# Kernel tuning notes

Measured on AMD Instinct MI355X. Metric: run time of the kernel, lower is better.

## Reference

```python
import jax, jax.numpy as jnp
import numpy as np


def setup_inputs() -> dict:
    key = jax.random.key(0)
    k1, k2 = jax.random.split(key)
    B, S, D, E = 4, 4096, 2048, 64
    x = jax.random.normal(k1, (B, S, D), dtype=jnp.float32)
    gate_w = jax.random.normal(k2, (E, D), dtype=jnp.float32) * (1.0 / np.sqrt(D))
    return {"x": x, "gate_w": gate_w, "top_k": 2}


def reference(x, gate_w, top_k):
    # logits = x @ W^T : [B, S, E]
    logits = jnp.einsum("bsd,ed->bse", x, gate_w)
    probs = jax.nn.softmax(logits, axis=-1)
    top_k_probs, top_k_indices = jax.lax.top_k(probs, top_k)
    top_k_probs = top_k_probs / jnp.sum(top_k_probs, axis=-1, keepdims=True)
    return (top_k_probs, top_k_indices, probs)
```

## Files before the change

### kernel.cpp

```cpp
#include <hip/hip_runtime.h>
#include <math.h>


typedef _Float16 half8  __attribute__((ext_vector_type(8)));
typedef float    floatx4 __attribute__((ext_vector_type(4)));

#define NTOK  16384
#define DDIM  2048
#define NE    64

__device__ inline void split8(const float4& a, const float4& b,
                              half8& hi, half8& lo) {
    float f[8] = {a.x, a.y, a.z, a.w, b.x, b.y, b.z, b.w};
#pragma unroll
    for (int j = 0; j < 8; ++j) {
        const _Float16 h = (_Float16)f[j];
        hi[j] = h;
        lo[j] = (_Float16)(f[j] - (float)h);
    }
}

__global__ __launch_bounds__(256) void w_split2(const float* __restrict__ W,
                                                _Float16* __restrict__ img) {
    const int g  = blockIdx.x * 256 + threadIdx.x;
    const int L  = g & 63;
    const int Bk = g >> 6;
    const int h  = Bk & 1;
    const int nt = (Bk >> 1) & 3;
    const int ch = (Bk >> 3) & 1;
    const int gs = Bk >> 4;
    const int c  = L & 15, q = L >> 4;
    const float* src = W + (size_t)(nt * 16 + c) * DDIM
                         + gs * 64 + ch * 32 + q * 8;
    const float4 a = *(const float4*)(src);
    const float4 b = *(const float4*)(src + 4);
    half8 hi, lo;
    split8(a, b, hi, lo);
    *(half8*)(img + (size_t)g * 8) = h ? lo : hi;
}

__global__ __launch_bounds__(256, 3) void router_mfma(
    const float* __restrict__ x,
    const _Float16* __restrict__ img,
    float* __restrict__ out)
{
    __shared__ __align__(16) float lg[4 * 16 * 68];

    const int tid = threadIdx.x;
    const int L   = tid & 63;
    const int kq  = __builtin_amdgcn_readfirstlane(tid >> 6);
    const int c   = L & 15, q = L >> 4;
    const int btok = blockIdx.x * 16;

    const float*    xp = x + (size_t)(btok + c) * DDIM + kq * 512 + q * 8;
    const _Float16* wp = img + (size_t)kq * 65536 + (size_t)L * 8;

    floatx4 acc[4];
#pragma unroll
    for (int nt = 0; nt < 4; ++nt) acc[nt] = (floatx4)0.f;

    float4 xA[4], xB[4];

    auto LX = [&](int s, float4* xb) {
#pragma unroll
        for (int ch = 0; ch < 2; ++ch) {
            xb[2 * ch + 0] = *(const float4*)(xp + s * 64 + ch * 32);
            xb[2 * ch + 1] = *(const float4*)(xp + s * 64 + ch * 32 + 4);
        }
    };
    auto LW = [&](int s, half8* wb) {
#pragma unroll
        for (int f = 0; f < 16; ++f)
            wb[f] = *(const half8*)(wp + (size_t)s * 8192 + f * 512);
    };
    auto CP = [&](const float4* xb, const half8* wb) {
#pragma unroll
        for (int ch = 0; ch < 2; ++ch) {
            half8 Ah, Al;
            split8(xb[2 * ch], xb[2 * ch + 1], Ah, Al);
#pragma unroll
            for (int nt = 0; nt < 4; ++nt) {
                const half8 Bh = wb[ch * 8 + nt * 2];
                const half8 Bl = wb[ch * 8 + nt * 2 + 1];
                acc[nt] = __builtin_amdgcn_mfma_f32_16x16x32_f16(Ah, Bh, acc[nt], 0, 0, 0);
                acc[nt] = __builtin_amdgcn_mfma_f32_16x16x32_f16(Al, Bh, acc[nt], 0, 0, 0);
                acc[nt] = __builtin_amdgcn_mfma_f32_16x16x32_f16(Ah, Bl, acc[nt], 0, 0, 0);
            }
        }
    };

    LX(0, xA);
    LX(1, xB);
#pragma unroll 1
    for (int b = 0; b < 6; b += 2) {
        half8 wA[16], wB[16];
        LW(b, wA);
        CP(xA, wA);
        LX(b + 2, xA);
        LW(b + 1, wB);
        CP(xB, wB);
        LX(b + 3, xB);
    }
    {
        half8 wA[16], wB[16];
        LW(6, wA); CP(xA, wA);
        LW(7, wB); CP(xB, wB);
    }

    {
        float* slab = &lg[kq * 16 * 68];
#pragma unroll
        for (int nt = 0; nt < 4; ++nt)
#pragma unroll
            for (int r = 0; r < 4; ++r)
                slab[(q * 4 + r) * 68 + nt * 16 + c] = acc[nt][r];
    }
    __syncthreads();

#pragma unroll
    for (int i = 0; i < 4; ++i) {
        const int e = tid + 256 * i;
        const int r = e >> 6, col = e & 63;
        const int o = r * 68 + col;
        lg[o] = (lg[o] + lg[1088 + o]) + (lg[2176 + o] + lg[3264 + o]);
    }
    __syncthreads();

    if (tid < 16) {
        const int token = btok + tid;
        float* row = &lg[tid * 68];
        float pr[NE];
#pragma unroll
        for (int e = 0; e < NE; ++e) pr[e] = row[e];

        float m = pr[0];
#pragma unroll
        for (int e = 1; e < NE; ++e) m = fmaxf(m, pr[e]);
        float s = 0.f;
#pragma unroll
        for (int e = 0; e < NE; ++e) { pr[e] = expf(pr[e] - m); s += pr[e]; }
        const float inv = 1.f / s;

        float v1 = -1.f; int i1 = 0;
#pragma unroll
        for (int e = 0; e < NE; ++e) { if (pr[e] > v1) { v1 = pr[e]; i1 = e; } }
        float v2 = -1.f; int i2 = 0;
#pragma unroll
        for (int e = 0; e < NE; ++e) { if (e != i1 && pr[e] > v2) { v2 = pr[e]; i2 = e; } }

        const float ts = v1 + v2;
        float* out_tp = out;
        float* out_ti = out + 2 * NTOK;
        *(float2*)(out_tp + token * 2) = make_float2(v1 / ts, v2 / ts);
        *(float2*)(out_ti + token * 2) = make_float2((float)i1, (float)i2);

#pragma unroll
        for (int e = 0; e < NE; ++e) row[e] = pr[e] * inv;
    }
    __syncthreads();

    {
        float* out_p = out + 4 * NTOK + (size_t)btok * NE;
        const int r = tid >> 4, c4 = tid & 15;
        const float4 v = *(const float4*)&lg[r * 68 + 4 * c4];
        *(float4*)(out_p + tid * 4) = v;
    }
}

extern "C" void kernel_launch(void* const* d_in, const int* in_sizes, int n_in,
                              void* d_out, int out_size, void* d_ws, size_t ws_size,
                              hipStream_t stream) {
    const float* x = (const float*)d_in[0];
    const float* W = (const float*)d_in[1];
    float* out     = (float*)d_out;
    _Float16* img  = (_Float16*)d_ws;

    w_split2<<<dim3(128), dim3(256), 0, stream>>>(W, img);
    router_mfma<<<dim3(NTOK / 16), dim3(256), 0, stream>>>(x, img, out);
}
```

Measured before the change: 206.1 us.

## Fuse weight split into router kernel with LDS double-buffered 32-token tiles

Removes the separate weight-split pre-kernel. Each block now loads fp32 W and x slices from global memory per K-step, splits them into fp16 hi/lo parts, and stages them in double-buffered LDS. The block grows to 512 threads covering 32 tokens, with each wave owning one 16x16 output tile, so the cross-wave K-reduction through shared memory goes away. In exchange, every block re-reads and re-splits all of W, and each K-step pays a block-wide barrier with little prefetch depth.

```diff
diff --git a/kernel.cpp b/kernel.cpp
--- a/kernel.cpp
+++ b/kernel.cpp
@@ -3,11 +3,14 @@
 
 
 typedef _Float16 half8  __attribute__((ext_vector_type(8)));
+typedef _Float16 half4  __attribute__((ext_vector_type(4)));
 typedef float    floatx4 __attribute__((ext_vector_type(4)));
 
 #define NTOK  16384
 #define DDIM  2048
 #define NE    64
+#define TPB   32
+#define NSTEP 32
 
 __device__ inline void split8(const float4& a, const float4& b,
                               half8& hi, half8& lo) {
@@ -20,113 +23,103 @@
     }
 }
 
-__global__ __launch_bounds__(256) void w_split2(const float* __restrict__ W,
-                                                _Float16* __restrict__ img) {
-    const int g  = blockIdx.x * 256 + threadIdx.x;
-    const int L  = g & 63;
-    const int Bk = g >> 6;
-    const int h  = Bk & 1;
-    const int nt = (Bk >> 1) & 3;
-    const int ch = (Bk >> 3) & 1;
-    const int gs = Bk >> 4;
-    const int c  = L & 15, q = L >> 4;
-    const float* src = W + (size_t)(nt * 16 + c) * DDIM
-                         + gs * 64 + ch * 32 + q * 8;
-    const float4 a = *(const float4*)(src);
-    const float4 b = *(const float4*)(src + 4);
-    half8 hi, lo;
-    split8(a, b, hi, lo);
-    *(half8*)(img + (size_t)g * 8) = h ? lo : hi;
+__device__ inline void split4(const float4& a, half4& hi, half4& lo) {
+    float f[4] = {a.x, a.y, a.z, a.w};
+#pragma unroll
+    for (int j = 0; j < 4; ++j) {
+        const _Float16 h = (_Float16)f[j];
+        hi[j] = h;
+        lo[j] = (_Float16)(f[j] - (float)h);
+    }
 }
 
-__global__ __launch_bounds__(256, 3) void router_mfma(
+__global__ __launch_bounds__(512, 4) void router_one(
     const float* __restrict__ x,
-    const _Float16* __restrict__ img,
+    const float* __restrict__ W,
     float* __restrict__ out)
 {
-    __shared__ __align__(16) float lg[4 * 16 * 68];
+    __shared__ __align__(16) _Float16 tiles[2 * 12288];
+    __shared__ __align__(16) float lg[TPB * 68];
 
     const int tid = threadIdx.x;
     const int L   = tid & 63;
-    const int kq  = __builtin_amdgcn_readfirstlane(tid >> 6);
+    const int wv  = __builtin_amdgcn_readfirstlane(tid >> 6);
+    const int nh  = wv & 3;
+    const int tg  = wv >> 2;
     const int c   = L & 15, q = L >> 4;
-    const int btok = blockIdx.x * 16;
+    const int btok = blockIdx.x * TPB;
 
-    const float*    xp = x + (size_t)(btok + c) * DDIM + kq * 512 + q * 8;
-    const _Float16* wp = img + (size_t)kq * 65536 + (size_t)L * 8;
+    const int su_ch = tid >> 8, su_nt = (tid >> 6) & 3, su_l = tid & 63;
+    const float* wsrc = W + (size_t)(su_nt * 16 + (su_l & 15)) * DDIM
+                          + su_ch * 32 + (su_l >> 4) * 8;
+    const int w_off = tid * 8;
 
-    floatx4 acc[4];
+    const int sr = tid >> 4, hg = tid & 15;
+    const float* xsrc = x + (size_t)(btok + sr) * DDIM + hg * 4;
+    const int xg = hg >> 1, xh2 = hg & 1;
+    const int xdst = (sr * 8 + (xg ^ (sr & 7))) * 8 + xh2 * 4;
+
+    int aoff[2], boff[2];
 #pragma unroll
-    for (int nt = 0; nt < 4; ++nt) acc[nt] = (floatx4)0.f;
+    for (int ch = 0; ch < 2; ++ch) {
+        aoff[ch] = ((tg * 16 + c) * 8 + ((ch * 4 + q) ^ (c & 7))) * 8;
+        boff[ch] = ((ch * 4 + nh) * 64 + L) * 8;
+    }
 
-    float4 xA[4], xB[4];
+    floatx4 acc = (floatx4)0.f;
 
-    auto LX = [&](int s, float4* xb) {
+    auto stage = [&](int sel, const float4& wa, const float4& wb,
+                     const float4& xa) {
+        _Float16* nb = &tiles[sel * 12288];
+        half8 whi, wlo; split8(wa, wb, whi, wlo);
+        *(half8*)(nb + 4096 + w_off) = whi;
+        *(half8*)(nb + 8192 + w_off) = wlo;
+        half4 xhi, xlo; split4(xa, xhi, xlo);
+        *(half4*)(nb + xdst)        = xhi;
+        *(half4*)(nb + 2048 + xdst) = xlo;
+    };
+
+    auto compute = [&](int sel) {
+        const _Float16* base = &tiles[sel * 12288];
 #pragma unroll
         for (int ch = 0; ch < 2; ++ch) {
-            xb[2 * ch + 0] = *(const float4*)(xp + s * 64 + ch * 32);
-            xb[2 * ch + 1] = *(const float4*)(xp + s * 64 + ch * 32 + 4);
-        }
-    };
-    auto LW = [&](int s, half8* wb) {
-#pragma unroll
-        for (int f = 0; f < 16; ++f)
-            wb[f] = *(const half8*)(wp + (size_t)s * 8192 + f * 512);
-    };
-    auto CP = [&](const float4* xb, const half8* wb) {
-#pragma unroll
-        for (int ch = 0; ch < 2; ++ch) {
-            half8 Ah, Al;
-            split8(xb[2 * ch], xb[2 * ch + 1], Ah, Al);
-#pragma unroll
-            for (int nt = 0; nt < 4; ++nt) {
-                const half8 Bh = wb[ch * 8 + nt * 2];
-                const half8 Bl = wb[ch * 8 + nt * 2 + 1];
-                acc[nt] = __builtin_amdgcn_mfma_f32_16x16x32_f16(Ah, Bh, acc[nt], 0, 0, 0);
-                acc[nt] = __builtin_amdgcn_mfma_f32_16x16x32_f16(Al, Bh, acc[nt], 0, 0, 0);
-                acc[nt] = __builtin_amdgcn_mfma_f32_16x16x32_f16(Ah, Bl, acc[nt], 0, 0, 0);
-            }
+            const half8 Ah = *(const half8*)(base + aoff[ch]);
+            const half8 Al = *(const half8*)(base + 2048 + aoff[ch]);
+            const half8 Bh = *(const half8*)(base + 4096 + boff[ch]);
+            const half8 Bl = *(const half8*)(base + 8192 + boff[ch]);
+            acc = __builtin_amdgcn_mfma_f32_16x16x32_f16(Ah, Bh, acc, 0, 0, 0);
+            acc = __builtin_amdgcn_mfma_f32_16x16x32_f16(Al, Bh, acc, 0, 0, 0);
+            acc = __builtin_amdgcn_mfma_f32_16x16x32_f16(Ah, Bl, acc, 0, 0, 0);
         }
     };
 
-    LX(0, xA);
-    LX(1, xB);
-#pragma unroll 1
-    for (int b = 0; b < 6; b += 2) {
-        half8 wA[16], wB[16];
-        LW(b, wA);
-        CP(xA, wA);
-        LX(b + 2, xA);
-        LW(b + 1, wB);
-        CP(xB, wB);
-        LX(b + 3, xB);
-    }
     {
-        half8 wA[16], wB[16];
-        LW(6, wA); CP(xA, wA);
-        LW(7, wB); CP(xB, wB);
-    }
-
-    {
-        float* slab = &lg[kq * 16 * 68];
-#pragma unroll
-        for (int nt = 0; nt < 4; ++nt)
-#pragma unroll
-            for (int r = 0; r < 4; ++r)
-                slab[(q * 4 + r) * 68 + nt * 16 + c] = acc[nt][r];
+        const float4 wa = *(const float4*)(wsrc);
+        const float4 wb = *(const float4*)(wsrc + 4);
+        const float4 xa = *(const float4*)(xsrc);
+        stage(0, wa, wb, xa);
     }
     __syncthreads();
 
+    for (int t = 0; t < NSTEP; ++t) {
+        float4 wa, wb, xa;
+        if (t + 1 < NSTEP) {
+            wa = *(const float4*)(wsrc + (t + 1) * 64);
+            wb = *(const float4*)(wsrc + (t + 1) * 64 + 4);
+            xa = *(const float4*)(xsrc + (t + 1) * 64);
+        }
+        __builtin_amdgcn_sched_barrier(0);
+        compute(t & 1);
+        if (t + 1 < NSTEP) stage((t + 1) & 1, wa, wb, xa);
+        __syncthreads();
+    }
+
 #pragma unroll
-    for (int i = 0; i < 4; ++i) {
-        const int e = tid + 256 * i;
-        const int r = e >> 6, col = e & 63;
-        const int o = r * 68 + col;
-        lg[o] = (lg[o] + lg[1088 + o]) + (lg[2176 + o] + lg[3264 + o]);
-    }
+    for (int r = 0; r < 4; ++r)
+        lg[(tg * 16 + q * 4 + r) * 68 + nh * 16 + c] = acc[r];
     __syncthreads();
 
-    if (tid < 16) {
+    if (tid < TPB) {
         const int token = btok + tid;
         float* row = &lg[tid * 68];
         float pr[NE];
@@ -173,8 +166,7 @@
     const float* x = (const float*)d_in[0];
     const float* W = (const float*)d_in[1];
     float* out     = (float*)d_out;
-    _Float16* img  = (_Float16*)d_ws;
+    (void)d_ws; (void)ws_size;
 
-    w_split2<<<dim3(128), dim3(256), 0, stream>>>(W, img);
-    router_mfma<<<dim3(NTOK / 16), dim3(256), 0, stream>>>(x, img, out);
+    router_one<<<dim3(NTOK / TPB), dim3(512), 0, stream>>>(x, W, out);
 }
```

After: 204.0 us. Within noise of the previous version (-1.0%).
